# Performance work log

Hardware: AMD Instinct MI355X
Metric: run time of the kernel (lower is better)

## Reference

```python
import jax, jax.numpy as jnp
import numpy as np

EMBED_DIM = 1024
MODULE_DIM = 128
MODULE_COUNT = 128  # must equal MODULE_DIM for the original matmul to be valid
N_TOKENS = 16384


def setup_inputs() -> dict:
    key = jax.random.key(0)
    ks = jax.random.split(key, 9)
    s_e = 1.0 / np.sqrt(EMBED_DIM)
    s_d = 1.0 / np.sqrt(MODULE_DIM)
    return {
        "h0": jax.random.normal(ks[0], (N_TOKENS, EMBED_DIM), dtype=jnp.float32),
        "we0_w": jax.random.uniform(ks[1], (MODULE_DIM, EMBED_DIM), minval=-s_e, maxval=s_e, dtype=jnp.float32),
        "we0_b": jax.random.uniform(ks[2], (MODULE_DIM,), minval=-s_e, maxval=s_e, dtype=jnp.float32),
        "ws_w": jax.random.uniform(ks[3], (MODULE_COUNT, MODULE_DIM), minval=-s_d, maxval=s_d, dtype=jnp.float32),
        "ws_b": jax.random.uniform(ks[4], (MODULE_COUNT,), minval=-s_d, maxval=s_d, dtype=jnp.float32),
        "wm_w": jax.random.uniform(ks[5], (MODULE_COUNT, MODULE_DIM, MODULE_DIM), minval=-s_d, maxval=s_d, dtype=jnp.float32),
        "wm_b": jax.random.uniform(ks[6], (MODULE_COUNT, MODULE_DIM), minval=-s_d, maxval=s_d, dtype=jnp.float32),
        "we1_w": jax.random.uniform(ks[7], (EMBED_DIM, MODULE_DIM), minval=-s_d, maxval=s_d, dtype=jnp.float32),
        "we1_b": jax.random.uniform(ks[8], (EMBED_DIM,), minval=-s_d, maxval=s_d, dtype=jnp.float32),
    }


def reference(h0, we0_w, we0_b, ws_w, ws_b, wm_w, wm_b, we1_w, we1_b):
    # h0: [N, E]
    enc = h0 @ we0_w.T + we0_b                                   # [N, D]
    # stacked expert linears: acts[m, n, k] = relu(sum_d enc[n,d] * wm_w[m,k,d] + wm_b[m,k])
    acts = jax.nn.relu(jnp.einsum('nd,mkd->mnk', enc, wm_w) + wm_b[:, None, :])  # [M, N, D]
    # gating logits [N, M]; NOTE: softmax over dim 0 (the batch axis), faithful to original
    gate = jax.nn.softmax(enc @ ws_w.T + ws_b, axis=0)           # [N, M]
    # original: matmul(acts.transpose(0,1) [N,M,D], gate[...,None] [N,M,1]) with D == M
    # mixed[n, i] = sum_j acts[i, n, j] * gate[n, j]
    mixed = jnp.einsum('inj,nj->ni', acts, gate)                 # [N, M] (== [N, D])
    decoded = mixed @ we1_w.T + we1_b                            # [N, E]
    return jax.nn.relu(decoded + h0)
```

## Files before the change

### kernel.cpp

```cpp
#include <hip/hip_runtime.h>


#define N_TOK   16384
#define EMB     1024
#define MDIM    128

typedef __attribute__((ext_vector_type(8))) short   short8;
typedef __attribute__((ext_vector_type(4))) float   f32x4;
typedef __attribute__((ext_vector_type(4))) float   fv4;
typedef __attribute__((ext_vector_type(4))) unsigned short us4;

static __device__ __forceinline__ unsigned short f2bf(float f) {
    union { float f; unsigned u; } v; v.f = f;
    unsigned r = v.u + 0x7FFFu + ((v.u >> 16) & 1u);
    return (unsigned short)(r >> 16);
}
static __device__ __forceinline__ float bf2f_lo(unsigned u) {
    union { unsigned u; float f; } v; v.u = u << 16; return v.f;
}
static __device__ __forceinline__ float bf2f_hi(unsigned u) {
    union { unsigned u; float f; } v; v.u = u & 0xffff0000u; return v.f;
}

__global__ void k_convert_all(const float* __restrict__ wm_w,
                              const float* __restrict__ we0_w,
                              const float* __restrict__ we1_w,
                              const float* __restrict__ ws_w,
                              unsigned short* __restrict__ dst) {
    const int NFV4 = 593920;
    for (int i = blockIdx.x * blockDim.x + threadIdx.x; i < NFV4;
         i += gridDim.x * blockDim.x) {
        const float* src;
        if (i < 524288)       src = wm_w  + (size_t)i * 4;
        else if (i < 557056)  src = we0_w + (size_t)(i - 524288) * 4;
        else if (i < 589824)  src = we1_w + (size_t)(i - 557056) * 4;
        else                  src = ws_w  + (size_t)(i - 589824) * 4;
        fv4 v = *(const fv4*)src;
        us4 o;
        o.x = f2bf(v.x); o.y = f2bf(v.y); o.z = f2bf(v.z); o.w = f2bf(v.w);
        *(us4*)(dst + (size_t)i * 4) = o;
    }
}


__global__ __launch_bounds__(256) void k_enc(const float* __restrict__ h0,
                                             const unsigned short* __restrict__ we0b,
                                             const unsigned short* __restrict__ wsb,
                                             const float* __restrict__ we0_bias,
                                             const float* __restrict__ ws_bias,
                                             unsigned short* __restrict__ encT,
                                             float* __restrict__ logT) {
    __shared__ unsigned short Wt[128 * 128];
    __shared__ unsigned short Ht[32 * 128];
    __shared__ unsigned short Et[32 * 128];

    const int tid = threadIdx.x;
    const int lane = tid & 63, w = tid >> 6;
    const int c = lane & 15, g = lane >> 4;
    const int wd = w >> 1, wt = w & 1;
    const int t0 = blockIdx.x * 32;

    f32x4 acc[4] = {};
    for (int ks = 0; ks < 8; ++ks) {
        #pragma unroll
        for (int it = 0; it < 8; ++it) {
            int m = it * 256 + tid;
            int row = m >> 4, gc = m & 15;
            short8 v = *(const short8*)(we0b + row * 1024 + ks * 128 + gc * 8);
            *(short8*)&Wt[row * 128 + ((gc ^ (row & 7)) * 8)] = v;
        }
        #pragma unroll
        for (int it = 0; it < 2; ++it) {
            int m = it * 256 + tid;
            int row = m >> 4, gc = m & 15;
            const float* hp = h0 + (size_t)(t0 + row) * 1024 + ks * 128 + gc * 8;
            fv4 v0 = *(const fv4*)hp;
            fv4 v1 = *(const fv4*)(hp + 4);
            short8 ov;
            ov[0] = (short)f2bf(v0.x); ov[1] = (short)f2bf(v0.y);
            ov[2] = (short)f2bf(v0.z); ov[3] = (short)f2bf(v0.w);
            ov[4] = (short)f2bf(v1.x); ov[5] = (short)f2bf(v1.y);
            ov[6] = (short)f2bf(v1.z); ov[7] = (short)f2bf(v1.w);
            *(short8*)&Ht[row * 128 + ((gc ^ (row & 7)) * 8)] = ov;
        }
        __syncthreads();
        #pragma unroll
        for (int s = 0; s < 4; ++s) {
            int gk = s * 4 + g;
            int brow = wt * 16 + c;
            short8 b = *(const short8*)&Ht[brow * 128 + ((gk ^ (brow & 7)) * 8)];
            #pragma unroll
            for (int jf = 0; jf < 4; ++jf) {
                int j = wd * 64 + jf * 16 + c;
                short8 a = *(const short8*)&Wt[j * 128 + ((gk ^ (j & 7)) * 8)];
                acc[jf] = __builtin_amdgcn_mfma_f32_16x16x32_bf16(a, b, acc[jf], 0, 0, 0);
            }
        }
        __syncthreads();
    }
    const int tile = blockIdx.x * 2 + wt;
    const int erow = wt * 16 + c;
    #pragma unroll
    for (int f = 0; f < 4; ++f) {
        int d0 = wd * 64 + f * 16 + 4 * g;
        int s = wd * 2 + (f >> 1);
        int chunk = ((f & 1) ? 2 : 0) + (g >> 1);
        int e = (g & 1) * 4;
        fv4 bi = *(const fv4*)(we0_bias + d0);
        us4 o;
        o.x = f2bf(acc[f][0] + bi.x);
        o.y = f2bf(acc[f][1] + bi.y);
        o.z = f2bf(acc[f][2] + bi.z);
        o.w = f2bf(acc[f][3] + bi.w);
        *(us4*)(encT + (size_t)tile * 2048 + s * 512 + (chunk * 16 + c) * 8 + e) = o;
        int cg = d0 >> 3, off = d0 & 7;
        *(us4*)&Et[erow * 128 + ((cg ^ (erow & 7)) * 8) + off] = o;
    }
    __syncthreads();

    short8 al[4][4];
    #pragma unroll
    for (int jf = 0; jf < 4; ++jf)
        #pragma unroll
        for (int s = 0; s < 4; ++s)
            al[jf][s] = *(const short8*)(wsb + (wd * 64 + jf * 16 + c) * 128 + s * 32 + g * 8);
    short8 bl[4];
    #pragma unroll
    for (int s = 0; s < 4; ++s) {
        int cg2 = s * 4 + g;
        bl[s] = *(const short8*)&Et[erow * 128 + ((cg2 ^ (erow & 7)) * 8)];
    }
    f32x4 acc2[4] = {};
    #pragma unroll
    for (int s = 0; s < 4; ++s)
        #pragma unroll
        for (int jf = 0; jf < 4; ++jf)
            acc2[jf] = __builtin_amdgcn_mfma_f32_16x16x32_bf16(al[jf][s], bl[s], acc2[jf], 0, 0, 0);
    const int tokc = t0 + wt * 16 + c;
    #pragma unroll
    for (int jf = 0; jf < 4; ++jf) {
        int m0 = wd * 64 + jf * 16 + 4 * g;
        fv4 bs = *(const fv4*)(ws_bias + m0);
        logT[(size_t)(m0 + 0) * N_TOK + tokc] = acc2[jf][0] + bs.x;
        logT[(size_t)(m0 + 1) * N_TOK + tokc] = acc2[jf][1] + bs.y;
        logT[(size_t)(m0 + 2) * N_TOK + tokc] = acc2[jf][2] + bs.z;
        logT[(size_t)(m0 + 3) * N_TOK + tokc] = acc2[jf][3] + bs.w;
    }
}

__global__ __launch_bounds__(256) void k_softmax0(const float* __restrict__ logT,
                                                  unsigned short* __restrict__ gateT) {
    __shared__ float red[8];
    const int m = blockIdx.x;
    const int tid = threadIdx.x;
    const int lane = tid & 63, wv = tid >> 6;
    const float* row = logT + (size_t)m * N_TOK;

    fv4 v[16];
    float vmax = -3.0e38f;
    #pragma unroll
    for (int it = 0; it < 16; ++it) {
        v[it] = *(const fv4*)(row + it * 1024 + tid * 4);
        vmax = fmaxf(vmax, fmaxf(fmaxf(v[it].x, v[it].y), fmaxf(v[it].z, v[it].w)));
    }
    #pragma unroll
    for (int o = 32; o > 0; o >>= 1) vmax = fmaxf(vmax, __shfl_xor(vmax, o));
    if (lane == 0) red[wv] = vmax;
    __syncthreads();
    const float bmax = fmaxf(fmaxf(red[0], red[1]), fmaxf(red[2], red[3]));

    float s = 0.f;
    #pragma unroll
    for (int it = 0; it < 16; ++it) {
        v[it].x = __expf(v[it].x - bmax); v[it].y = __expf(v[it].y - bmax);
        v[it].z = __expf(v[it].z - bmax); v[it].w = __expf(v[it].w - bmax);
        s += v[it].x + v[it].y + v[it].z + v[it].w;
    }
    #pragma unroll
    for (int o = 32; o > 0; o >>= 1) s += __shfl_xor(s, o);
    if (lane == 0) red[4 + wv] = s;
    __syncthreads();
    const float inv = 1.f / (red[4] + red[5] + red[6] + red[7]);

    const int q  = m >> 5;
    const int w8 = ((m >> 4) & 1) * 4 + (m & 3);
    const int gl = ((m & 15) >> 2) * 16;
    #pragma unroll
    for (int it = 0; it < 16; ++it) {
        int t = it * 1024 + tid * 4;
        float pv[4] = { v[it].x * inv, v[it].y * inv, v[it].z * inv, v[it].w * inv };
        #pragma unroll
        for (int k = 0; k < 4; ++k) {
            int tok = t + k;
            gateT[(size_t)(tok >> 4) * 2048 + q * 512 + (gl + (tok & 15)) * 8 + w8] = f2bf(pv[k]);
        }
    }
}

__global__ __launch_bounds__(256)
__attribute__((amdgpu_waves_per_eu(2, 2)))
void k_mix(const unsigned short* __restrict__ wmb,
           const unsigned short* __restrict__ encT,
           const unsigned short* __restrict__ gateT,
           const float* __restrict__ wm_bias,
           unsigned short* __restrict__ mixT) {
    const int bid = blockIdx.x;
    const int i = bid & 127, tg = bid >> 7;
    const int tid = threadIdx.x;
    const int lane = tid & 63, w = tid >> 6;
    const int c = lane & 15, g = lane >> 4;

    const unsigned short* wmi = wmb + (size_t)i * 16384;
    short8 a[8][4];
    #pragma unroll
    for (int jf = 0; jf < 8; ++jf)
        #pragma unroll
        for (int s = 0; s < 4; ++s) {
            a[jf][s] = *(const short8*)(wmi + (jf * 16 + c) * 128 + s * 32 + g * 8);
            asm volatile("" : "+v"(a[jf][s]));
        }
    f32x4 bias4[8];
    #pragma unroll
    for (int f = 0; f < 8; ++f) {
        bias4[f] = *(const f32x4*)(wm_bias + i * 128 + f * 16 + 4 * g);
        asm volatile("" : "+v"(bias4[f]));
    }

    const int si = i >> 5, ch = (i & 31) >> 3, ei = i & 7;

    short8 b[4];
    {
        const unsigned short* ep = encT + (size_t)(tg * 128 + w) * 2048 + lane * 8;
        b[0] = *(const short8*)(ep);
        b[1] = *(const short8*)(ep + 512);
        b[2] = *(const short8*)(ep + 1024);
        b[3] = *(const short8*)(ep + 1536);
    }

    #pragma unroll 2
    for (int rr = 0; rr < 32; ++rr) {
        const int tile = tg * 128 + rr * 4 + w;
        const int nrr = (rr < 31) ? rr + 1 : 31;
        const unsigned short* epn = encT + (size_t)(tg * 128 + nrr * 4 + w) * 2048 + lane * 8;
        short8 nb0 = *(const short8*)(epn);
        short8 nb1 = *(const short8*)(epn + 512);
        short8 nb2 = *(const short8*)(epn + 1024);
        short8 nb3 = *(const short8*)(epn + 1536);
        const unsigned* gp = (const unsigned*)(gateT + (size_t)tile * 2048) + lane * 4;
        uint4 G0 = *(const uint4*)(gp);
        uint4 G1 = *(const uint4*)(gp + 256);
        uint4 G2 = *(const uint4*)(gp + 512);
        uint4 G3 = *(const uint4*)(gp + 768);

        f32x4 acc[8];
        #pragma unroll
        for (int jf = 0; jf < 8; ++jf)
            acc[jf] = __builtin_amdgcn_mfma_f32_16x16x32_bf16(a[jf][0], b[0], bias4[jf], 0, 0, 0);
        #pragma unroll
        for (int jf = 0; jf < 8; ++jf)
            acc[jf] = __builtin_amdgcn_mfma_f32_16x16x32_bf16(a[jf][1], b[1], acc[jf], 0, 0, 0);
        #pragma unroll
        for (int jf = 0; jf < 8; ++jf)
            acc[jf] = __builtin_amdgcn_mfma_f32_16x16x32_bf16(a[jf][2], b[2], acc[jf], 0, 0, 0);
        #pragma unroll
        for (int jf = 0; jf < 8; ++jf)
            acc[jf] = __builtin_amdgcn_mfma_f32_16x16x32_bf16(a[jf][3], b[3], acc[jf], 0, 0, 0);

        float p0 = 0.f, p1 = 0.f, p2 = 0.f, p3 = 0.f;
        #define EPI(F, GA, GB) {                                        \
            p0 += fmaxf(acc[F][0], 0.f) * bf2f_lo(GA);                  \
            p1 += fmaxf(acc[F][1], 0.f) * bf2f_hi(GA);                  \
            p2 += fmaxf(acc[F][2], 0.f) * bf2f_lo(GB);                  \
            p3 += fmaxf(acc[F][3], 0.f) * bf2f_hi(GB);                  \
        }
        EPI(0, G0.x, G0.y) EPI(1, G0.z, G0.w)
        EPI(2, G1.x, G1.y) EPI(3, G1.z, G1.w)
        EPI(4, G2.x, G2.y) EPI(5, G2.z, G2.w)
        EPI(6, G3.x, G3.y) EPI(7, G3.z, G3.w)
        #undef EPI
        float p = (p0 + p1) + (p2 + p3);
        p += __shfl_xor(p, 16);
        p += __shfl_xor(p, 32);
        if (lane < 16)
            mixT[(size_t)tile * 2048 + si * 512 + (ch * 16 + lane) * 8 + ei] = f2bf(p);

        b[0] = nb0; b[1] = nb1; b[2] = nb2; b[3] = nb3;
    }
}

__global__ __launch_bounds__(256)
__attribute__((amdgpu_waves_per_eu(2, 2)))
void k_dec(const unsigned short* __restrict__ we1b,
           const unsigned short* __restrict__ mixT,
           const float* __restrict__ we1_bias,
           const float* __restrict__ h0,
           float* __restrict__ out) {
    const int bid = blockIdx.x;
    const int eb = bid & 7, tg = bid >> 3;
    const int e0 = eb * 128;
    const int tid = threadIdx.x;
    const int lane = tid & 63, w = tid >> 6;
    const int c = lane & 15, g = lane >> 4;

    short8 a[8][4];
    #pragma unroll
    for (int jf = 0; jf < 8; ++jf)
        #pragma unroll
        for (int s = 0; s < 4; ++s) {
            a[jf][s] = *(const short8*)(we1b + (size_t)(e0 + jf * 16 + c) * 128 + s * 32 + g * 8);
            asm volatile("" : "+v"(a[jf][s]));
        }
    fv4 bi[8];
    #pragma unroll
    for (int f = 0; f < 8; ++f)
        bi[f] = *(const fv4*)(we1_bias + e0 + f * 16 + 4 * g);

    #pragma unroll 1
    for (int t = 0; t < 4; ++t) {
        const int tokr = tg * 256 + t * 64 + w * 16 + c;
        const int tile = tg * 16 + t * 4 + w;
        fv4 h[8];
        #pragma unroll
        for (int f = 0; f < 8; ++f)
            h[f] = *(const fv4*)(h0 + (size_t)tokr * 1024 + e0 + f * 16 + 4 * g);
        const unsigned short* mp = mixT + (size_t)tile * 2048 + lane * 8;
        short8 b[4];
        #pragma unroll
        for (int s = 0; s < 4; ++s)
            b[s] = *(const short8*)(mp + s * 512);

        f32x4 acc[8] = {};
        #pragma unroll
        for (int s = 0; s < 4; ++s)
            #pragma unroll
            for (int jf = 0; jf < 8; ++jf)
                acc[jf] = __builtin_amdgcn_mfma_f32_16x16x32_bf16(a[jf][s], b[s], acc[jf], 0, 0, 0);

        #pragma unroll
        for (int f = 0; f < 8; ++f) {
            fv4 o;
            o.x = fmaxf(acc[f][0] + bi[f].x + h[f].x, 0.f);
            o.y = fmaxf(acc[f][1] + bi[f].y + h[f].y, 0.f);
            o.z = fmaxf(acc[f][2] + bi[f].z + h[f].z, 0.f);
            o.w = fmaxf(acc[f][3] + bi[f].w + h[f].w, 0.f);
            *(fv4*)(out + (size_t)tokr * 1024 + e0 + f * 16 + 4 * g) = o;
        }
    }
}

extern "C" void kernel_launch(void* const* d_in, const int* in_sizes, int n_in,
                              void* d_out, int out_size, void* d_ws, size_t ws_size,
                              hipStream_t stream) {
    const float* h0    = (const float*)d_in[0];
    const float* we0_w = (const float*)d_in[1];
    const float* we0_b = (const float*)d_in[2];
    const float* ws_w  = (const float*)d_in[3];
    const float* ws_b  = (const float*)d_in[4];
    const float* wm_w  = (const float*)d_in[5];
    const float* wm_b  = (const float*)d_in[6];
    const float* we1_w = (const float*)d_in[7];
    const float* we1_b = (const float*)d_in[8];
    float* out = (float*)d_out;

    unsigned short* wmb   = (unsigned short*)d_ws;
    unsigned short* we0b  = wmb  + 2097152;
    unsigned short* we1b  = we0b + 131072;
    unsigned short* wsb   = we1b + 131072;
    unsigned short* encT  = wsb  + 16384;
    float*          logT  = (float*)(encT + 2097152);
    unsigned short* gateT = (unsigned short*)(logT + 2097152);
    unsigned short* mixT  = gateT + 2097152;

    k_convert_all<<<640, 256, 0, stream>>>(wm_w, we0_w, we1_w, ws_w, wmb);
    k_enc<<<512, 256, 0, stream>>>(h0, we0b, wsb, we0_b, ws_b, encT, logT);
    k_softmax0<<<128, 256, 0, stream>>>(logT, gateT);
    k_mix<<<1024, 256, 0, stream>>>(wmb, encT, gateT, wm_b, mixT);
    k_dec<<<512, 256, 0, stream>>>(we1b, mixT, we1_b, h0, out);
}
```

Measured before the change: 185.6 us.

## Halve mix grid, double tokens per block, drop software prefetch

The k_mix grid is halved to 512 blocks, so each block now covers 256 tokens (64 iterations) for one expert instead of 128. Block ids are remapped so that consecutive blocks share the same expert index i, which improves L2 locality of that expert's weights. The double-buffered encT prefetch and the asm register pins on the bias are removed, and the loop is no longer unrolled. This lowers register pressure and halves how often the per-block weights are loaded, but loses the load/MFMA overlap that prefetching gave. It also leaves fewer blocks to fill the CUs.

```diff
diff --git a/kernel.cpp b/kernel.cpp
--- a/kernel.cpp
+++ b/kernel.cpp
@@ -205,7 +205,7 @@
            const float* __restrict__ wm_bias,
            unsigned short* __restrict__ mixT) {
     const int bid = blockIdx.x;
-    const int i = bid & 127, tg = bid >> 7;
+    const int tg = bid & 3, i = bid >> 2;
     const int tid = threadIdx.x;
     const int lane = tid & 63, w = tid >> 6;
     const int c = lane & 15, g = lane >> 4;
@@ -221,31 +221,19 @@
         }
     f32x4 bias4[8];
     #pragma unroll
-    for (int f = 0; f < 8; ++f) {
+    for (int f = 0; f < 8; ++f)
         bias4[f] = *(const f32x4*)(wm_bias + i * 128 + f * 16 + 4 * g);
-        asm volatile("" : "+v"(bias4[f]));
-    }
 
     const int si = i >> 5, ch = (i & 31) >> 3, ei = i & 7;
 
-    short8 b[4];
-    {
-        const unsigned short* ep = encT + (size_t)(tg * 128 + w) * 2048 + lane * 8;
-        b[0] = *(const short8*)(ep);
-        b[1] = *(const short8*)(ep + 512);
-        b[2] = *(const short8*)(ep + 1024);
-        b[3] = *(const short8*)(ep + 1536);
-    }
-
-    #pragma unroll 2
-    for (int rr = 0; rr < 32; ++rr) {
-        const int tile = tg * 128 + rr * 4 + w;
-        const int nrr = (rr < 31) ? rr + 1 : 31;
-        const unsigned short* epn = encT + (size_t)(tg * 128 + nrr * 4 + w) * 2048 + lane * 8;
-        short8 nb0 = *(const short8*)(epn);
-        short8 nb1 = *(const short8*)(epn + 512);
-        short8 nb2 = *(const short8*)(epn + 1024);
-        short8 nb3 = *(const short8*)(epn + 1536);
+    #pragma unroll 1
+    for (int rr = 0; rr < 64; ++rr) {
+        const int tile = tg * 256 + rr * 4 + w;
+        const unsigned short* ep = encT + (size_t)tile * 2048 + lane * 8;
+        short8 b0 = *(const short8*)(ep);
+        short8 b1 = *(const short8*)(ep + 512);
+        short8 b2 = *(const short8*)(ep + 1024);
+        short8 b3 = *(const short8*)(ep + 1536);
         const unsigned* gp = (const unsigned*)(gateT + (size_t)tile * 2048) + lane * 4;
         uint4 G0 = *(const uint4*)(gp);
         uint4 G1 = *(const uint4*)(gp + 256);
@@ -255,16 +243,16 @@
         f32x4 acc[8];
         #pragma unroll
         for (int jf = 0; jf < 8; ++jf)
-            acc[jf] = __builtin_amdgcn_mfma_f32_16x16x32_bf16(a[jf][0], b[0], bias4[jf], 0, 0, 0);
+            acc[jf] = __builtin_amdgcn_mfma_f32_16x16x32_bf16(a[jf][0], b0, bias4[jf], 0, 0, 0);
         #pragma unroll
         for (int jf = 0; jf < 8; ++jf)
-            acc[jf] = __builtin_amdgcn_mfma_f32_16x16x32_bf16(a[jf][1], b[1], acc[jf], 0, 0, 0);
+            acc[jf] = __builtin_amdgcn_mfma_f32_16x16x32_bf16(a[jf][1], b1, acc[jf], 0, 0, 0);
         #pragma unroll
         for (int jf = 0; jf < 8; ++jf)
-            acc[jf] = __builtin_amdgcn_mfma_f32_16x16x32_bf16(a[jf][2], b[2], acc[jf], 0, 0, 0);
+            acc[jf] = __builtin_amdgcn_mfma_f32_16x16x32_bf16(a[jf][2], b2, acc[jf], 0, 0, 0);
         #pragma unroll
         for (int jf = 0; jf < 8; ++jf)
-            acc[jf] = __builtin_amdgcn_mfma_f32_16x16x32_bf16(a[jf][3], b[3], acc[jf], 0, 0, 0);
+            acc[jf] = __builtin_amdgcn_mfma_f32_16x16x32_bf16(a[jf][3], b3, acc[jf], 0, 0, 0);
 
         float p0 = 0.f, p1 = 0.f, p2 = 0.f, p3 = 0.f;
         #define EPI(F, GA, GB) {                                        \
@@ -283,8 +271,6 @@
         p += __shfl_xor(p, 32);
         if (lane < 16)
             mixT[(size_t)tile * 2048 + si * 512 + (ch * 16 + lane) * 8 + ei] = f2bf(p);
-
-        b[0] = nb0; b[1] = nb1; b[2] = nb2; b[3] = nb3;
     }
 }
 
@@ -374,6 +360,6 @@
     k_convert_all<<<640, 256, 0, stream>>>(wm_w, we0_w, we1_w, ws_w, wmb);
     k_enc<<<512, 256, 0, stream>>>(h0, we0b, wsb, we0_b, ws_b, encT, logT);
     k_softmax0<<<128, 256, 0, stream>>>(logT, gateT);
-    k_mix<<<1024, 256, 0, stream>>>(wmb, encT, gateT, wm_b, mixT);
+    k_mix<<<512, 256, 0, stream>>>(wmb, encT, gateT, wm_b, mixT);
     k_dec<<<512, 256, 0, stream>>>(we1b, mixT, we1_b, h0, out);
 }
```

Result: faster. 173.9 us (-6.3%).
